# Optimization experiments

Hardware: AMD Instinct MI355X
Metric: run time of the kernel (lower is better)

## Reference

```python
import jax, jax.numpy as jnp
import numpy as np

# DBMLLoss hyperparameters (from cfg.LOSSES.DBML_LOSS.*)
POS_A, POS_B = 1.0, 0.5
NEG_A, NEG_B = 0.6, 0.5
MARGIN, WEIGHT = 0.1, 0.5
EPS = 1e-5


def setup_inputs() -> dict:
    key = jax.random.key(0)
    k1, k2 = jax.random.split(key)
    feats = jax.random.normal(k1, (4096, 512), dtype=jnp.float32)
    feats = feats / jnp.linalg.norm(feats, axis=1, keepdims=True)  # metric-learning embeddings are L2-normalized
    labels = jax.random.randint(k2, (4096,), 0, 100)
    return {"feats": feats, "labels": labels}


def _dbml_loss(feats, labels):
    # feats: [B, D], labels: [B] int
    B = feats.shape[0]
    ninf = jnp.array(-jnp.inf, feats.dtype)
    pinf = jnp.array(jnp.inf, feats.dtype)

    sim = feats @ feats.T  # [B, B]
    same = labels[:, None] == labels[None, :]  # [B, B]
    # pos_pair_: same label and sim < 1 - eps (drops self-similarity of normalized feats)
    pos_mask = same & (sim < 1.0 - EPS)
    neg_mask = ~same

    # full-row stats (torch.mean(sum(...)) over a scalar == the sum)
    mean_all = sim.mean(axis=1)                               # [B]
    sigma_all = ((sim - mean_all[:, None]) ** 2).sum(axis=1)  # [B]

    max_neg = jnp.max(jnp.where(neg_mask, sim, ninf), axis=1)  # [B]
    min_pos = jnp.min(jnp.where(pos_mask, sim, pinf), axis=1)  # [B]

    # adaptive selection (adaptive_neg=True branch)
    pos_sel = pos_mask & (sim - MARGIN < max_neg[:, None])
    neg_sel = neg_mask & (sim + MARGIN > min_pos[:, None])

    n_pos = pos_sel.sum(axis=1)
    n_neg = neg_sel.sum(axis=1)
    valid = (pos_mask.sum(axis=1) > 0) & (neg_mask.sum(axis=1) > 0) & (n_pos > 0) & (n_neg > 0)

    sel = pos_sel | neg_sel
    cnt = jnp.maximum(n_pos + n_neg, 1).astype(sim.dtype)     # guard div-by-0 on invalid rows
    mean_sel = jnp.where(sel, sim, 0.0).sum(axis=1) / cnt
    sigma_sel = jnp.where(sel, (sim - mean_sel[:, None]) ** 2, 0.0).sum(axis=1) / cnt

    # fp = 1 + sum exp(-(pos - pos_a)/pos_b); fn = 1 + sum exp((neg - neg_a)/neg_b)
    fp = 1.0 + jnp.exp(jnp.where(pos_sel, -(sim - POS_A) / POS_B, ninf)).sum(axis=1)
    fn = 1.0 + jnp.exp(jnp.where(neg_sel, (sim - NEG_A) / NEG_B, ninf)).sum(axis=1)

    loss_i = (jnp.log(fp) + jnp.log(fn)
              + WEIGHT * (jnp.abs(mean_all - mean_sel) + jnp.abs(sigma_all - sigma_sel)))
    return jnp.where(valid, loss_i, 0.0).sum() / B


def reference(feats, labels):
    return _dbml_loss(feats, labels)
```

## Files before the change

kernel.cpp:

```cpp
#include <hip/hip_runtime.h>
#include <stdint.h>


#define Bn 4096
#define Dk 512
#define NCHUNK 16
#define CWIDTH 256
#define BM 128
#define TBN 128
#define BK 64
#define NSTEP 16
#define ONE_EPS 0.99999f

typedef short bf16x8 __attribute__((ext_vector_type(8)));
typedef unsigned short u16x4 __attribute__((ext_vector_type(4)));
typedef float f32x4 __attribute__((ext_vector_type(4)));

__device__ __forceinline__ unsigned short f2bf(float x) {
  unsigned int u = __float_as_uint(x);
  u += 0x7fffu + ((u >> 16) & 1u);
  return (unsigned short)(u >> 16);
}

__global__ __launch_bounds__(256) void convert_kernel(const float* __restrict__ feats,
                                                      unsigned short* __restrict__ featT) {
  int g = blockIdx.x * 256 + threadIdx.x;
  int row = g & 4095;
  int kb = g >> 12;
  const float* src = feats + (size_t)row * Dk + kb * 8;
  f32x4 f0 = *(const f32x4*)(src);
  f32x4 f1 = *(const f32x4*)(src + 4);
  union { unsigned short u[8]; bf16x8 v; } o;
  o.u[0] = f2bf(f0[0]); o.u[1] = f2bf(f0[1]); o.u[2] = f2bf(f0[2]); o.u[3] = f2bf(f0[3]);
  o.u[4] = f2bf(f1[0]); o.u[5] = f2bf(f1[1]); o.u[6] = f2bf(f1[2]); o.u[7] = f2bf(f1[3]);
  *(bf16x8*)(featT + (size_t)g * 8) = o.v;
}

__device__ __forceinline__ void gload16(const unsigned short* g, short* l) {
  __builtin_amdgcn_global_load_lds((const __attribute__((address_space(1))) unsigned int*)g,
                                   (__attribute__((address_space(3))) unsigned int*)l,
                                   16, 0, 0);
}

template <int PHASE, bool WSIM>
__global__ __launch_bounds__(512, 2) void phase_kernel(const unsigned short* __restrict__ featT,
                                                       const int* __restrict__ labels,
                                                       const float* __restrict__ rs,
                                                       float* __restrict__ part,
                                                       unsigned short* __restrict__ simb) {
  __shared__ short As[2][8192];
  __shared__ short Bs[2][8192];
  __shared__ int rl[BM];
  __shared__ int cl[CWIDTH];

  const int tid = threadIdx.x;
  const int wid = tid >> 6;
  const int lane = tid & 63;
  const int WR = wid & 3;
  const int WC = wid >> 2;
  const int l15 = lane & 15;
  const int l4 = lane >> 4;
  const int row0 = blockIdx.x * BM;
  const int chunk0 = blockIdx.y * CWIDTH;

  if (tid < BM) rl[tid] = labels[row0 + tid];
  if (tid < CWIDTH) cl[tid] = labels[chunk0 + tid];

  int rlab[2][4], rowl[2][4];
  float thrp[2][4], thrn[2][4];
#pragma unroll
  for (int m = 0; m < 2; ++m)
#pragma unroll
    for (int r = 0; r < 4; ++r) {
      int lr = WR * 32 + m * 16 + l4 * 4 + r;
      rowl[m][r] = lr;
      rlab[m][r] = 0;
      if constexpr (PHASE == 2) {
        thrp[m][r] = rs[2 * Bn + row0 + lr];
        thrn[m][r] = rs[3 * Bn + row0 + lr];
      }
    }

  float s0[2][4], s1[2][4], s2[2][4], s3[2][4], s4[2][4], s5[2][4];
#pragma unroll
  for (int m = 0; m < 2; ++m)
#pragma unroll
    for (int r = 0; r < 4; ++r) {
      s0[m][r] = 0.f; s1[m][r] = 0.f;
      s2[m][r] = (PHASE == 1) ? -__builtin_inff() : 0.f;
      s3[m][r] = (PHASE == 1) ? __builtin_inff() : 0.f;
      s4[m][r] = 0.f; s5[m][r] = 0.f;
    }

  auto stage = [&](int s) {
    const int ct = s >> 3, kt = s & 7, bb = s & 1;
    const int cbase = chunk0 + ct * TBN;
#pragma unroll
    for (int i = 0; i < 2; ++i) {
      const int q = tid + i * 512;
      const int r = q & 127;
      const int kb = q >> 7;
      const int ko = (kt * 8 + kb) * (Bn * 8);
      gload16(featT + ko + (row0 + r) * 8, &As[bb][q * 8]);
      gload16(featT + ko + (cbase + r) * 8, &Bs[bb][q * 8]);
    }
  };

  stage(0);

  for (int ct = 0; ct < CWIDTH / TBN; ++ct) {
    const int col0 = chunk0 + ct * TBN;
    f32x4 acc[2][4];
#pragma unroll
    for (int m = 0; m < 2; ++m)
#pragma unroll
      for (int n = 0; n < 4; ++n) acc[m][n] = (f32x4){0.f, 0.f, 0.f, 0.f};

    for (int kt = 0; kt < Dk / BK; ++kt) {
      const int s = ct * 8 + kt;
      __syncthreads();
      if (s + 1 < NSTEP) stage(s + 1);
      if (s == 0) {
#pragma unroll
        for (int m = 0; m < 2; ++m)
#pragma unroll
          for (int r = 0; r < 4; ++r) rlab[m][r] = rl[rowl[m][r]];
      }
      const int bb = s & 1;
#pragma unroll
      for (int ks = 0; ks < 2; ++ks) {
        const int kb = ks * 4 + l4;
        bf16x8 af[2], bf[4];
#pragma unroll
        for (int m = 0; m < 2; ++m)
          af[m] = *(const bf16x8*)&As[bb][(kb * 128 + WR * 32 + m * 16 + l15) * 8];
#pragma unroll
        for (int n = 0; n < 4; ++n)
          bf[n] = *(const bf16x8*)&Bs[bb][(kb * 128 + WC * 64 + n * 16 + l15) * 8];
#pragma unroll
        for (int m = 0; m < 2; ++m)
#pragma unroll
          for (int n = 0; n < 4; ++n)
            acc[m][n] = __builtin_amdgcn_mfma_f32_16x16x32_bf16(af[m], bf[n], acc[m][n], 0, 0, 0);
      }
    }

    const bool diag = (col0 == row0);
#pragma unroll
    for (int n = 0; n < 4; ++n) {
      const int lcolt = WC * 64 + n * 16 + l15;
      const int clab = cl[ct * TBN + lcolt];
#pragma unroll
      for (int m = 0; m < 2; ++m) {
        float tv[4];
#pragma unroll
        for (int r = 0; r < 4; ++r) {
          float s = acc[m][n][r];
          if (diag && (lcolt == rowl[m][r])) s = 1.0f;
          tv[r] = s;
        }
        if constexpr (WSIM) {
          u16x4 w;
#pragma unroll
          for (int r = 0; r < 4; ++r) w[r] = f2bf(tv[r]);
          *(u16x4*)(simb + (size_t)(col0 + lcolt) * Bn +
                    (row0 + WR * 32 + m * 16 + l4 * 4)) = w;
        }
#pragma unroll
        for (int r = 0; r < 4; ++r) {
          float s = tv[r];
          bool same = (rlab[m][r] == clab);
          if constexpr (PHASE == 1) {
            s0[m][r] += s;
            s1[m][r] += s * s;
            if (!same) s2[m][r] = fmaxf(s2[m][r], s);
            else if (s < ONE_EPS) { s3[m][r] = fminf(s3[m][r], s); s4[m][r] += 1.0f; }
          } else {
            bool psel = same && (s < ONE_EPS) && (s - 0.1f < thrp[m][r]);
            bool nsel = (!same) && (s + 0.1f > thrn[m][r]);
            if (psel) { s0[m][r] += 1.0f; s4[m][r] += __expf(2.0f - 2.0f * s); }
            if (nsel) { s1[m][r] += 1.0f; s5[m][r] += __expf(2.0f * s - 1.2f); }
            if (psel || nsel) { s2[m][r] += s; s3[m][r] += s * s; }
          }
        }
      }
    }
  }

#pragma unroll
  for (int d = 1; d < 16; d <<= 1) {
#pragma unroll
    for (int m = 0; m < 2; ++m)
#pragma unroll
      for (int r = 0; r < 4; ++r) {
        s0[m][r] += __shfl_xor(s0[m][r], d);
        s1[m][r] += __shfl_xor(s1[m][r], d);
        if constexpr (PHASE == 1) {
          s2[m][r] = fmaxf(s2[m][r], __shfl_xor(s2[m][r], d));
          s3[m][r] = fminf(s3[m][r], __shfl_xor(s3[m][r], d));
          s4[m][r] += __shfl_xor(s4[m][r], d);
        } else {
          s2[m][r] += __shfl_xor(s2[m][r], d);
          s3[m][r] += __shfl_xor(s3[m][r], d);
          s4[m][r] += __shfl_xor(s4[m][r], d);
          s5[m][r] += __shfl_xor(s5[m][r], d);
        }
      }
  }

  __syncthreads();
  float* mbuf = (float*)&As[0][0];
  if (WC == 1 && l15 == 0) {
#pragma unroll
    for (int m = 0; m < 2; ++m)
#pragma unroll
      for (int r = 0; r < 4; ++r) {
        int lr = rowl[m][r];
        mbuf[lr * 6 + 0] = s0[m][r];
        mbuf[lr * 6 + 1] = s1[m][r];
        mbuf[lr * 6 + 2] = s2[m][r];
        mbuf[lr * 6 + 3] = s3[m][r];
        mbuf[lr * 6 + 4] = s4[m][r];
        mbuf[lr * 6 + 5] = s5[m][r];
      }
  }
  __syncthreads();
  if (WC == 0 && l15 == 0) {
    const int slot = blockIdx.y;
#pragma unroll
    for (int m = 0; m < 2; ++m)
#pragma unroll
      for (int r = 0; r < 4; ++r) {
        int lr = rowl[m][r];
        int rowg = row0 + lr;
        const float* p = &mbuf[lr * 6];
        float t0 = s0[m][r] + p[0];
        float t1 = s1[m][r] + p[1];
        float t2, t3;
        if constexpr (PHASE == 1) {
          t2 = fmaxf(s2[m][r], p[2]);
          t3 = fminf(s3[m][r], p[3]);
        } else {
          t2 = s2[m][r] + p[2];
          t3 = s3[m][r] + p[3];
        }
        float t4 = s4[m][r] + p[4];
        part[(size_t)(0 * Bn + rowg) * 16 + slot] = t0;
        part[(size_t)(1 * Bn + rowg) * 16 + slot] = t1;
        part[(size_t)(2 * Bn + rowg) * 16 + slot] = t2;
        part[(size_t)(3 * Bn + rowg) * 16 + slot] = t3;
        part[(size_t)(4 * Bn + rowg) * 16 + slot] = t4;
        if constexpr (PHASE == 2)
          part[(size_t)(5 * Bn + rowg) * 16 + slot] = s5[m][r] + p[5];
      }
  }
}

__global__ __launch_bounds__(512) void pass2_kernel(const unsigned short* __restrict__ simb,
                                                    const int* __restrict__ labels,
                                                    const float* __restrict__ p1,
                                                    float* __restrict__ out) {
  __shared__ int cl[Bn];
  __shared__ float bs[8];
  const int tid = threadIdx.x;
  for (int i = tid; i < Bn / 4; i += 512) ((int4*)cl)[i] = ((const int4*)labels)[i];
  __syncthreads();
  const int lane = tid & 63;
  const int wv = tid >> 6;
  const int row = blockIdx.x * 8 + wv;
  const int rlab = cl[row];

  const int sl = lane & 15;
  float ssum = p1[(size_t)(0 * Bn + row) * 16 + sl];
  float sssq = p1[(size_t)(1 * Bn + row) * 16 + sl];
  float smxn = p1[(size_t)(2 * Bn + row) * 16 + sl];
  float smnp = p1[(size_t)(3 * Bn + row) * 16 + sl];
  float spc  = p1[(size_t)(4 * Bn + row) * 16 + sl];
#pragma unroll
  for (int d = 1; d < 16; d <<= 1) {
    ssum += __shfl_xor(ssum, d);
    sssq += __shfl_xor(sssq, d);
    smxn = fmaxf(smxn, __shfl_xor(smxn, d));
    smnp = fminf(smnp, __shfl_xor(smnp, d));
    spc += __shfl_xor(spc, d);
  }
  const float thrp = smxn;
  const float thrn = smnp;

  float np = 0.f, nn = 0.f, ssel = 0.f, qsel = 0.f, fp = 0.f, fn = 0.f;
  const unsigned short* rp = simb + (size_t)row * Bn;
#pragma unroll
  for (int it = 0; it < 8; ++it) {
    const int base = it * 512 + lane * 8;
    bf16x8 v = *(const bf16x8*)(rp + base);
    int4 la = *(const int4*)&cl[base];
    int4 lb = *(const int4*)&cl[base + 4];
    int lv[8] = {la.x, la.y, la.z, la.w, lb.x, lb.y, lb.z, lb.w};
#pragma unroll
    for (int e = 0; e < 8; ++e) {
      float s = __uint_as_float(((unsigned int)(unsigned short)v[e]) << 16);
      bool same = (lv[e] == rlab);
      bool psel = same && (s < ONE_EPS) && (s - 0.1f < thrp);
      bool nsel = (!same) && (s + 0.1f > thrn);
      if (psel) { np += 1.f; fp += __expf(2.0f - 2.0f * s); }
      if (nsel) { nn += 1.f; fn += __expf(2.0f * s - 1.2f); }
      if (psel || nsel) { ssel += s; qsel += s * s; }
    }
  }
#pragma unroll
  for (int d = 1; d < 64; d <<= 1) {
    np += __shfl_xor(np, d); nn += __shfl_xor(nn, d);
    ssel += __shfl_xor(ssel, d); qsel += __shfl_xor(qsel, d);
    fp += __shfl_xor(fp, d); fn += __shfl_xor(fn, d);
  }

  float mean_all = ssum * (1.0f / Bn);
  float sigma_all = sssq - (float)Bn * mean_all * mean_all;
  float cnt = fmaxf(np + nn, 1.0f);
  float mean_sel = ssel / cnt;
  float sigma_sel = qsel / cnt - mean_sel * mean_sel;
  float loss = __logf(1.0f + fp) + __logf(1.0f + fn) +
               0.5f * (fabsf(mean_all - mean_sel) + fabsf(sigma_all - sigma_sel));
  bool valid = (spc > 0.5f) && (spc < (float)(Bn - 1) - 0.5f) && (np > 0.5f) && (nn > 0.5f);
  float v0 = valid ? loss : 0.f;

  if (lane == 0) bs[wv] = v0;
  __syncthreads();
  if (tid == 0) {
    float t = bs[0] + bs[1] + bs[2] + bs[3] + bs[4] + bs[5] + bs[6] + bs[7];
    atomicAdd(out, t * (1.0f / (float)Bn));
  }
}

__global__ __launch_bounds__(256) void reduce1_kernel(const float* __restrict__ part,
                                                      float* __restrict__ rs) {
  int row = blockIdx.x * 256 + threadIdx.x;
  float sum = 0.f, ssq = 0.f, pc = 0.f;
  float mxn = -__builtin_inff(), mnp = __builtin_inff();
#pragma unroll
  for (int sl = 0; sl < 16; ++sl) {
    sum += part[(size_t)(0 * Bn + row) * 16 + sl];
    ssq += part[(size_t)(1 * Bn + row) * 16 + sl];
    mxn = fmaxf(mxn, part[(size_t)(2 * Bn + row) * 16 + sl]);
    mnp = fminf(mnp, part[(size_t)(3 * Bn + row) * 16 + sl]);
    pc += part[(size_t)(4 * Bn + row) * 16 + sl];
  }
  rs[0 * Bn + row] = sum;
  rs[1 * Bn + row] = ssq;
  rs[2 * Bn + row] = mxn;
  rs[3 * Bn + row] = mnp;
  rs[4 * Bn + row] = pc;
}

__global__ __launch_bounds__(256) void finalize_kernel(const float* __restrict__ p2,
                                                       const float* __restrict__ rs,
                                                       float* __restrict__ out) {
  int tid = threadIdx.x;
  int row = blockIdx.x * 256 + tid;
  float np = 0.f, nn = 0.f, ssel = 0.f, qsel = 0.f, fp = 0.f, fn = 0.f;
#pragma unroll
  for (int sl = 0; sl < 16; ++sl) {
    np += p2[(size_t)(0 * Bn + row) * 16 + sl];
    nn += p2[(size_t)(1 * Bn + row) * 16 + sl];
    ssel += p2[(size_t)(2 * Bn + row) * 16 + sl];
    qsel += p2[(size_t)(3 * Bn + row) * 16 + sl];
    fp += p2[(size_t)(4 * Bn + row) * 16 + sl];
    fn += p2[(size_t)(5 * Bn + row) * 16 + sl];
  }
  float sumall = rs[0 * Bn + row];
  float ssqall = rs[1 * Bn + row];
  float pc = rs[4 * Bn + row];

  float mean_all = sumall * (1.0f / Bn);
  float sigma_all = ssqall - (float)Bn * mean_all * mean_all;
  float cnt = fmaxf(np + nn, 1.0f);
  float mean_sel = ssel / cnt;
  float sigma_sel = qsel / cnt - mean_sel * mean_sel;
  float loss = __logf(1.0f + fp) + __logf(1.0f + fn) +
               0.5f * (fabsf(mean_all - mean_sel) + fabsf(sigma_all - sigma_sel));
  bool valid = (pc > 0.5f) && (pc < (float)(Bn - 1) - 0.5f) && (np > 0.5f) && (nn > 0.5f);
  float v = valid ? loss : 0.f;
#pragma unroll
  for (int d = 1; d < 64; d <<= 1) v += __shfl_xor(v, d);
  __shared__ float ls[4];
  if ((tid & 63) == 0) ls[tid >> 6] = v;
  __syncthreads();
  if (tid == 0) atomicAdd(out, (ls[0] + ls[1] + ls[2] + ls[3]) * (1.0f / (float)Bn));
}

extern "C" void kernel_launch(void* const* d_in, const int* in_sizes, int n_in,
                              void* d_out, int out_size, void* d_ws, size_t ws_size,
                              hipStream_t stream) {
  const float* feats = (const float*)d_in[0];
  const int* labels = (const int*)d_in[1];
  float* out = (float*)d_out;
  char* ws = (char*)d_ws;

  unsigned short* featT = (unsigned short*)ws;
  float* p1 = (float*)(ws + 4194304);
  const size_t needA = 4194304ull + 1310720ull + 33554432ull;

  hipMemsetAsync(d_out, 0, sizeof(float), stream);
  convert_kernel<<<1024, 256, 0, stream>>>(feats, featT);
  dim3 g(Bn / BM, NCHUNK);

  if (ws_size >= needA) {
    unsigned short* simb = (unsigned short*)(ws + 4194304 + 1310720);
    phase_kernel<1, true><<<g, 512, 0, stream>>>(featT, labels, nullptr, p1, simb);
    pass2_kernel<<<512, 512, 0, stream>>>(simb, labels, p1, out);
  } else {
    float* rs = (float*)(ws + 4194304 + 1310720);
    float* p2 = (float*)(ws + 4194304 + 1310720 + 81920);
    phase_kernel<1, false><<<g, 512, 0, stream>>>(featT, labels, nullptr, p1, nullptr);
    reduce1_kernel<<<Bn / 256, 256, 0, stream>>>(p1, rs);
    phase_kernel<2, false><<<g, 512, 0, stream>>>(featT, labels, rs, p2, nullptr);
    finalize_kernel<<<Bn / 256, 256, 0, stream>>>(p2, rs, out);
  }
}
```

Measured before the change: 125.7 us.

## Deepen GEMM prefetch pipeline with explicit waitcnt and halve pass2 block size

Rewrites the phase kernel main loop into a single 16-step loop that keeps two stages of global-to-LDS loads in flight, using explicit vmcnt/lgkmcnt waits and raw barriers in place of __syncthreads. Source and destination addresses are precomputed once, and the epilogue fold for the first column tile runs mid-loop. This aims to hide load latency behind MFMA work and cut address arithmetic. pass2 now uses 256-thread blocks handling 4 rows each, doubling the grid size. The hand-written waitcnt counts are fragile and rely on exact knowledge of how many loads are outstanding.

```diff
diff --git a/kernel.cpp b/kernel.cpp
--- a/kernel.cpp
+++ b/kernel.cpp
@@ -8,8 +8,6 @@
 #define CWIDTH 256
 #define BM 128
 #define TBN 128
-#define BK 64
-#define NSTEP 16
 #define ONE_EPS 0.99999f
 
 typedef short bf16x8 __attribute__((ext_vector_type(8)));
@@ -63,8 +61,34 @@
   const int row0 = blockIdx.x * BM;
   const int chunk0 = blockIdx.y * CWIDTH;
 
+  const unsigned short* aSrc[2]; const unsigned short* bSrc[2];
+  short* aDst[2]; short* bDst[2];
+#pragma unroll
+  for (int i = 0; i < 2; ++i) {
+    const int q = tid + i * 512;
+    const int r = q & 127;
+    const int kb = q >> 7;
+    aSrc[i] = featT + ((size_t)kb * Bn + row0 + r) * 8;
+    bSrc[i] = featT + ((size_t)kb * Bn + chunk0 + r) * 8;
+    aDst[i] = &As[0][0] + q * 8;
+    bDst[i] = &Bs[0][0] + q * 8;
+  }
+  auto stage = [&](int s) {
+    const int kt = s & 7, ct = s >> 3, bb = s & 1;
+    const size_t ko = (size_t)kt * 262144;
+#pragma unroll
+    for (int i = 0; i < 2; ++i) {
+      gload16(aSrc[i] + ko, aDst[i] + bb * 8192);
+      gload16(bSrc[i] + ko + ct * 1024, bDst[i] + bb * 8192);
+    }
+  };
+
+  stage(0);
+  stage(1);
+
   if (tid < BM) rl[tid] = labels[row0 + tid];
   if (tid < CWIDTH) cl[tid] = labels[chunk0 + tid];
+  asm volatile("s_waitcnt lgkmcnt(0)" ::: "memory");
 
   int rlab[2][4], rowl[2][4];
   float thrp[2][4], thrn[2][4];
@@ -92,59 +116,17 @@
       s4[m][r] = 0.f; s5[m][r] = 0.f;
     }
 
-  auto stage = [&](int s) {
-    const int ct = s >> 3, kt = s & 7, bb = s & 1;
-    const int cbase = chunk0 + ct * TBN;
-#pragma unroll
-    for (int i = 0; i < 2; ++i) {
-      const int q = tid + i * 512;
-      const int r = q & 127;
-      const int kb = q >> 7;
-      const int ko = (kt * 8 + kb) * (Bn * 8);
-      gload16(featT + ko + (row0 + r) * 8, &As[bb][q * 8]);
-      gload16(featT + ko + (cbase + r) * 8, &Bs[bb][q * 8]);
-    }
-  };
-
-  stage(0);
-
-  for (int ct = 0; ct < CWIDTH / TBN; ++ct) {
+  f32x4 acc[2][4];
+#pragma unroll
+  for (int m = 0; m < 2; ++m)
+#pragma unroll
+    for (int n = 0; n < 4; ++n) acc[m][n] = (f32x4){0.f, 0.f, 0.f, 0.f};
+
+  const int aFixed = l4 * 1024 + WR * 256 + l15 * 8;
+  const int bFixed = l4 * 1024 + WC * 512 + l15 * 8;
+
+  auto fold = [&](int ct) {
     const int col0 = chunk0 + ct * TBN;
-    f32x4 acc[2][4];
-#pragma unroll
-    for (int m = 0; m < 2; ++m)
-#pragma unroll
-      for (int n = 0; n < 4; ++n) acc[m][n] = (f32x4){0.f, 0.f, 0.f, 0.f};
-
-    for (int kt = 0; kt < Dk / BK; ++kt) {
-      const int s = ct * 8 + kt;
-      __syncthreads();
-      if (s + 1 < NSTEP) stage(s + 1);
-      if (s == 0) {
-#pragma unroll
-        for (int m = 0; m < 2; ++m)
-#pragma unroll
-          for (int r = 0; r < 4; ++r) rlab[m][r] = rl[rowl[m][r]];
-      }
-      const int bb = s & 1;
-#pragma unroll
-      for (int ks = 0; ks < 2; ++ks) {
-        const int kb = ks * 4 + l4;
-        bf16x8 af[2], bf[4];
-#pragma unroll
-        for (int m = 0; m < 2; ++m)
-          af[m] = *(const bf16x8*)&As[bb][(kb * 128 + WR * 32 + m * 16 + l15) * 8];
-#pragma unroll
-        for (int n = 0; n < 4; ++n)
-          bf[n] = *(const bf16x8*)&Bs[bb][(kb * 128 + WC * 64 + n * 16 + l15) * 8];
-#pragma unroll
-        for (int m = 0; m < 2; ++m)
-#pragma unroll
-          for (int n = 0; n < 4; ++n)
-            acc[m][n] = __builtin_amdgcn_mfma_f32_16x16x32_bf16(af[m], bf[n], acc[m][n], 0, 0, 0);
-      }
-    }
-
     const bool diag = (col0 == row0);
 #pragma unroll
     for (int n = 0; n < 4; ++n) {
@@ -185,7 +167,48 @@
         }
       }
     }
-  }
+  };
+
+  for (int s = 0; s < 16; ++s) {
+    if (s < 15) asm volatile("s_waitcnt vmcnt(4)" ::: "memory");
+    else        asm volatile("s_waitcnt vmcnt(0)" ::: "memory");
+    __builtin_amdgcn_s_barrier();
+    if (s == 0) {
+#pragma unroll
+      for (int m = 0; m < 2; ++m)
+#pragma unroll
+        for (int r = 0; r < 4; ++r) rlab[m][r] = rl[rowl[m][r]];
+    }
+    const int bb = s & 1;
+    const short* Ab = &As[0][0] + bb * 8192 + aFixed;
+    const short* Bb = &Bs[0][0] + bb * 8192 + bFixed;
+#pragma unroll
+    for (int ks = 0; ks < 2; ++ks) {
+      bf16x8 af[2], bf[4];
+#pragma unroll
+      for (int m = 0; m < 2; ++m)
+        af[m] = *(const bf16x8*)(Ab + ks * 4096 + m * 128);
+#pragma unroll
+      for (int n = 0; n < 4; ++n)
+        bf[n] = *(const bf16x8*)(Bb + ks * 4096 + n * 128);
+#pragma unroll
+      for (int m = 0; m < 2; ++m)
+#pragma unroll
+        for (int n = 0; n < 4; ++n)
+          acc[m][n] = __builtin_amdgcn_mfma_f32_16x16x32_bf16(af[m], bf[n], acc[m][n], 0, 0, 0);
+    }
+    asm volatile("s_waitcnt lgkmcnt(0)" ::: "memory");
+    __builtin_amdgcn_s_barrier();
+    if (s + 2 < 16) stage(s + 2);
+    if (s == 7) {
+      fold(0);
+#pragma unroll
+      for (int m = 0; m < 2; ++m)
+#pragma unroll
+        for (int n = 0; n < 4; ++n) acc[m][n] = (f32x4){0.f, 0.f, 0.f, 0.f};
+    }
+  }
+  fold(1);
 
 #pragma unroll
   for (int d = 1; d < 16; d <<= 1) {
@@ -256,18 +279,18 @@
   }
 }
 
-__global__ __launch_bounds__(512) void pass2_kernel(const unsigned short* __restrict__ simb,
+__global__ __launch_bounds__(256) void pass2_kernel(const unsigned short* __restrict__ simb,
                                                     const int* __restrict__ labels,
                                                     const float* __restrict__ p1,
                                                     float* __restrict__ out) {
   __shared__ int cl[Bn];
-  __shared__ float bs[8];
+  __shared__ float bs[4];
   const int tid = threadIdx.x;
-  for (int i = tid; i < Bn / 4; i += 512) ((int4*)cl)[i] = ((const int4*)labels)[i];
+  for (int i = tid; i < Bn / 4; i += 256) ((int4*)cl)[i] = ((const int4*)labels)[i];
   __syncthreads();
   const int lane = tid & 63;
   const int wv = tid >> 6;
-  const int row = blockIdx.x * 8 + wv;
+  const int row = blockIdx.x * 4 + wv;
   const int rlab = cl[row];
 
   const int sl = lane & 15;
@@ -326,10 +349,7 @@
 
   if (lane == 0) bs[wv] = v0;
   __syncthreads();
-  if (tid == 0) {
-    float t = bs[0] + bs[1] + bs[2] + bs[3] + bs[4] + bs[5] + bs[6] + bs[7];
-    atomicAdd(out, t * (1.0f / (float)Bn));
-  }
+  if (tid == 0) atomicAdd(out, (bs[0] + bs[1] + bs[2] + bs[3]) * (1.0f / (float)Bn));
 }
 
 __global__ __launch_bounds__(256) void reduce1_kernel(const float* __restrict__ part,
@@ -407,7 +427,7 @@
   if (ws_size >= needA) {
     unsigned short* simb = (unsigned short*)(ws + 4194304 + 1310720);
     phase_kernel<1, true><<<g, 512, 0, stream>>>(featT, labels, nullptr, p1, simb);
-    pass2_kernel<<<512, 512, 0, stream>>>(simb, labels, p1, out);
+    pass2_kernel<<<Bn / 4, 256, 0, stream>>>(simb, labels, p1, out);
   } else {
     float* rs = (float*)(ws + 4194304 + 1310720);
     float* p2 = (float*)(ws + 4194304 + 1310720 + 81920);
```

Result: slower. 131.0 us (+4.3%).

## Split pass2 rows across waves and replace atomic with deterministic sum kernel

Applied to the files above, without the earlier changes.

pass2 now uses one 256-thread block per row instead of one wave per row. The four waves each scan a quarter of the row and combine their partial statistics through shared memory. The 16 KB label staging in LDS is dropped in favour of direct global loads, and the per-block atomicAdd is replaced by per-row results plus a single-block sum kernel, which also removes the memset on the fast path. This trades more blocks and an extra small launch for better parallelism and no atomics.

```diff
diff --git a/kernel.cpp b/kernel.cpp
--- a/kernel.cpp
+++ b/kernel.cpp
@@ -256,19 +256,16 @@
   }
 }
 
-__global__ __launch_bounds__(512) void pass2_kernel(const unsigned short* __restrict__ simb,
+__global__ __launch_bounds__(256) void pass2_kernel(const unsigned short* __restrict__ simb,
                                                     const int* __restrict__ labels,
                                                     const float* __restrict__ p1,
-                                                    float* __restrict__ out) {
-  __shared__ int cl[Bn];
-  __shared__ float bs[8];
+                                                    float* __restrict__ bres) {
+  __shared__ float red[4][6];
   const int tid = threadIdx.x;
-  for (int i = tid; i < Bn / 4; i += 512) ((int4*)cl)[i] = ((const int4*)labels)[i];
-  __syncthreads();
   const int lane = tid & 63;
   const int wv = tid >> 6;
-  const int row = blockIdx.x * 8 + wv;
-  const int rlab = cl[row];
+  const int row = blockIdx.x;
+  const int rlab = labels[row];
 
   const int sl = lane & 15;
   float ssum = p1[(size_t)(0 * Bn + row) * 16 + sl];
@@ -290,11 +287,11 @@
   float np = 0.f, nn = 0.f, ssel = 0.f, qsel = 0.f, fp = 0.f, fn = 0.f;
   const unsigned short* rp = simb + (size_t)row * Bn;
 #pragma unroll
-  for (int it = 0; it < 8; ++it) {
-    const int base = it * 512 + lane * 8;
+  for (int it = 0; it < 2; ++it) {
+    const int base = wv * 1024 + it * 512 + lane * 8;
     bf16x8 v = *(const bf16x8*)(rp + base);
-    int4 la = *(const int4*)&cl[base];
-    int4 lb = *(const int4*)&cl[base + 4];
+    int4 la = *(const int4*)&labels[base];
+    int4 lb = *(const int4*)&labels[base + 4];
     int lv[8] = {la.x, la.y, la.z, la.w, lb.x, lb.y, lb.z, lb.w};
 #pragma unroll
     for (int e = 0; e < 8; ++e) {
@@ -313,23 +310,43 @@
     ssel += __shfl_xor(ssel, d); qsel += __shfl_xor(qsel, d);
     fp += __shfl_xor(fp, d); fn += __shfl_xor(fn, d);
   }
-
-  float mean_all = ssum * (1.0f / Bn);
-  float sigma_all = sssq - (float)Bn * mean_all * mean_all;
-  float cnt = fmaxf(np + nn, 1.0f);
-  float mean_sel = ssel / cnt;
-  float sigma_sel = qsel / cnt - mean_sel * mean_sel;
-  float loss = __logf(1.0f + fp) + __logf(1.0f + fn) +
-               0.5f * (fabsf(mean_all - mean_sel) + fabsf(sigma_all - sigma_sel));
-  bool valid = (spc > 0.5f) && (spc < (float)(Bn - 1) - 0.5f) && (np > 0.5f) && (nn > 0.5f);
-  float v0 = valid ? loss : 0.f;
-
-  if (lane == 0) bs[wv] = v0;
+  if (lane == 0) {
+    red[wv][0] = np; red[wv][1] = nn; red[wv][2] = ssel;
+    red[wv][3] = qsel; red[wv][4] = fp; red[wv][5] = fn;
+  }
   __syncthreads();
   if (tid == 0) {
-    float t = bs[0] + bs[1] + bs[2] + bs[3] + bs[4] + bs[5] + bs[6] + bs[7];
-    atomicAdd(out, t * (1.0f / (float)Bn));
-  }
+    np = red[0][0] + red[1][0] + red[2][0] + red[3][0];
+    nn = red[0][1] + red[1][1] + red[2][1] + red[3][1];
+    ssel = red[0][2] + red[1][2] + red[2][2] + red[3][2];
+    qsel = red[0][3] + red[1][3] + red[2][3] + red[3][3];
+    fp = red[0][4] + red[1][4] + red[2][4] + red[3][4];
+    fn = red[0][5] + red[1][5] + red[2][5] + red[3][5];
+
+    float mean_all = ssum * (1.0f / Bn);
+    float sigma_all = sssq - (float)Bn * mean_all * mean_all;
+    float cnt = fmaxf(np + nn, 1.0f);
+    float mean_sel = ssel / cnt;
+    float sigma_sel = qsel / cnt - mean_sel * mean_sel;
+    float loss = __logf(1.0f + fp) + __logf(1.0f + fn) +
+                 0.5f * (fabsf(mean_all - mean_sel) + fabsf(sigma_all - sigma_sel));
+    bool valid = (spc > 0.5f) && (spc < (float)(Bn - 1) - 0.5f) && (np > 0.5f) && (nn > 0.5f);
+    bres[row] = valid ? loss : 0.f;
+  }
+}
+
+__global__ __launch_bounds__(256) void sum_kernel(const float* __restrict__ bres,
+                                                  float* __restrict__ out) {
+  const int tid = threadIdx.x;
+  float v = 0.f;
+#pragma unroll
+  for (int i = 0; i < 16; ++i) v += bres[i * 256 + tid];
+#pragma unroll
+  for (int d = 1; d < 64; d <<= 1) v += __shfl_xor(v, d);
+  __shared__ float ls[4];
+  if ((tid & 63) == 0) ls[tid >> 6] = v;
+  __syncthreads();
+  if (tid == 0) out[0] = (ls[0] + ls[1] + ls[2] + ls[3]) * (1.0f / (float)Bn);
 }
 
 __global__ __launch_bounds__(256) void reduce1_kernel(const float* __restrict__ part,
@@ -398,19 +415,21 @@
 
   unsigned short* featT = (unsigned short*)ws;
   float* p1 = (float*)(ws + 4194304);
-  const size_t needA = 4194304ull + 1310720ull + 33554432ull;
-
-  hipMemsetAsync(d_out, 0, sizeof(float), stream);
+  const size_t needA = 4194304ull + 1310720ull + 33554432ull + 16384ull;
+
   convert_kernel<<<1024, 256, 0, stream>>>(feats, featT);
   dim3 g(Bn / BM, NCHUNK);
 
   if (ws_size >= needA) {
     unsigned short* simb = (unsigned short*)(ws + 4194304 + 1310720);
+    float* bres = (float*)(ws + 4194304 + 1310720 + 33554432);
     phase_kernel<1, true><<<g, 512, 0, stream>>>(featT, labels, nullptr, p1, simb);
-    pass2_kernel<<<512, 512, 0, stream>>>(simb, labels, p1, out);
+    pass2_kernel<<<Bn, 256, 0, stream>>>(simb, labels, p1, bres);
+    sum_kernel<<<1, 256, 0, stream>>>(bres, out);
   } else {
     float* rs = (float*)(ws + 4194304 + 1310720);
     float* p2 = (float*)(ws + 4194304 + 1310720 + 81920);
+    hipMemsetAsync(d_out, 0, sizeof(float), stream);
     phase_kernel<1, false><<<g, 512, 0, stream>>>(featT, labels, nullptr, p1, nullptr);
     reduce1_kernel<<<Bn / 256, 256, 0, stream>>>(p1, rs);
     phase_kernel<2, false><<<g, 512, 0, stream>>>(featT, labels, rs, p2, nullptr);
```

Result: faster. 122.2 us (-2.8%).
